# Kernel optimization log

Measured on AMD Instinct MI355X. Metric: run time of the kernel, lower is better.

## Reference

```python
import jax, jax.numpy as jnp
import numpy as np

D, H, KVH, HD, FF = 768, 12, 4, 64, 2048
N_REP = H // KVH
EPS = 1e-6


def rmsnorm(x, w):
    # Faithful to source: norm = ||x|| * n^{-1/2}; eps added to norm (not inside sqrt)
    norm = jnp.sqrt(jnp.sum(x * x, axis=-1, keepdims=True)) * (x.shape[-1] ** -0.5)
    return w * x / (norm + EPS)


def rope_tables(seq_len, head_dim, base=10000.0):
    inv_freq = 1.0 / (base ** (np.arange(0, head_dim, 2, dtype=np.float32) / head_dim))
    t = np.arange(seq_len, dtype=np.float32)
    freqs = np.einsum('i,j->ij', t, inv_freq)  # [S, HD/2]
    emb = np.concatenate([freqs, freqs], axis=-1)  # [S, HD]
    return jnp.asarray(np.cos(emb)), jnp.asarray(np.sin(emb))


def rotate_half(x):
    h = x.shape[-1] // 2
    return jnp.concatenate([-x[..., h:], x[..., :h]], axis=-1)


def setup_inputs() -> dict:
    key = jax.random.key(0)
    ks = jax.random.split(key, 9)
    s = 0.02
    return {
        'x': jax.random.normal(ks[0], (2, 2048, D), jnp.float32),
        'Wq': jax.random.normal(ks[1], (H * HD, D), jnp.float32) * s,
        'Wk': jax.random.normal(ks[2], (KVH * HD, D), jnp.float32) * s,
        'Wv': jax.random.normal(ks[3], (KVH * HD, D), jnp.float32) * s,
        'Wo': jax.random.normal(ks[4], (D, H * HD), jnp.float32) * s,
        'Wgate': jax.random.normal(ks[5], (FF, D), jnp.float32) * s,
        'Wup': jax.random.normal(ks[6], (FF, D), jnp.float32) * s,
        'Wdown': jax.random.normal(ks[7], (D, FF), jnp.float32) * s,
        'g1': jnp.ones((D,), jnp.float32),
        'g2': jnp.ones((D,), jnp.float32),
    }


def reference(x, Wq, Wk, Wv, Wo, Wgate, Wup, Wdown, g1, g2):
    B, S, _ = x.shape
    # ---- attention sublayer (pre-norm) ----
    xn = rmsnorm(x, g1)
    q = (xn @ Wq.T).reshape(B, S, H, HD).transpose(0, 2, 1, 3)      # [B,H,S,HD]
    k = (xn @ Wk.T).reshape(B, S, KVH, HD).transpose(0, 2, 1, 3)    # [B,KVH,S,HD]
    v = (xn @ Wv.T).reshape(B, S, KVH, HD).transpose(0, 2, 1, 3)
    cos, sin = rope_tables(S, HD)                                   # [S,HD]
    q = q * cos + rotate_half(q) * sin
    k = k * cos + rotate_half(k) * sin
    # repeat kv heads to match q heads
    k = jnp.repeat(k, N_REP, axis=1)                                # [B,H,S,HD]
    v = jnp.repeat(v, N_REP, axis=1)
    scores = jnp.einsum('bhqd,bhkd->bhqk', q, k) / jnp.sqrt(jnp.float32(HD))
    causal = jnp.tril(jnp.ones((S, S), bool))
    scores = jnp.where(causal, scores, jnp.finfo(scores.dtype).min)
    attn = jax.nn.softmax(scores, axis=-1)
    out = jnp.einsum('bhqk,bhkd->bhqd', attn, v)                    # [B,H,S,HD]
    out = out.transpose(0, 2, 1, 3).reshape(B, S, H * HD) @ Wo.T
    x = x + out
    # ---- SwiGLU FFN sublayer (pre-norm) ----
    xn2 = rmsnorm(x, g2)
    ff = (jax.nn.silu(xn2 @ Wgate.T) * (xn2 @ Wup.T)) @ Wdown.T
    return x + ff
```

## Files before the change

### kernel.cpp

```cpp
#include <hip/hip_runtime.h>
#include <hip/hip_bf16.h>
#include <math.h>

typedef __bf16 bf16;
typedef __attribute__((ext_vector_type(8))) __bf16 bf16x8;
typedef __attribute__((ext_vector_type(4))) __bf16 bf16x4;
typedef __attribute__((ext_vector_type(4))) float f32x4;

#define MFMA16(a,b,c) __builtin_amdgcn_mfma_f32_16x16x32_bf16(a,b,c,0,0,0)

#define BATCH 2
#define SEQ   2048
#define DMODEL 768
#define NH    12
#define NKV   4
#define NREP  3
#define HD    64
#define FFDIM 2048
#define ROWS  (BATCH*SEQ)

#define QSCALE 0.18033688011112042f
#define LOG2E  1.4426950408889634f

#define WB(N) asm volatile("s_waitcnt vmcnt(" #N ")\n\ts_barrier" ::: "memory")
#define BAR() asm volatile("s_barrier" ::: "memory")

__device__ __forceinline__ void gl2lds16(const bf16* g, bf16* l) {
  __builtin_amdgcn_global_load_lds(
      (const __attribute__((address_space(1))) void*)g,
      (__attribute__((address_space(3))) void*)l, 16, 0, 0);
}

struct Cvt7 { const float* s[7]; bf16* d[7]; int n[7]; float* tab; };
__global__ __launch_bounds__(256) void cvt_all_kernel(Cvt7 c) {
  int seg = blockIdx.y;
  if (seg == 7) {
    int id = blockIdx.x * 256 + threadIdx.x;
    int j = id >> 11, s = id & 2047;
    float inv = expf(-(float)j * (9.210340371976184f / 32.0f));
    float ang = (float)s * inv;
    c.tab[id] = cosf(ang);
    c.tab[65536 + id] = sinf(ang);
    return;
  }
  const float* __restrict__ src = c.s[seg];
  bf16* __restrict__ dst = c.d[seg];
  int n = c.n[seg];
  int stride = gridDim.x * 256;
  for (int i = blockIdx.x * 256 + threadIdx.x; i < n; i += stride)
    dst[i] = (bf16)src[i];
}

__global__ __launch_bounds__(192) void rmsnorm_kernel(const float* __restrict__ x,
    const float* __restrict__ g, bf16* __restrict__ out) {
  int row = blockIdx.x;
  const float* xr = x + (size_t)row * DMODEL;
  int t = threadIdx.x;
  f32x4 v = *(const f32x4*)(xr + t * 4);
  float ss = v[0] * v[0] + v[1] * v[1] + v[2] * v[2] + v[3] * v[3];
  #pragma unroll
  for (int off = 32; off; off >>= 1) ss += __shfl_xor(ss, off, 64);
  __shared__ float red[3];
  if ((t & 63) == 0) red[t >> 6] = ss;
  __syncthreads();
  float total = red[0] + red[1] + red[2];
  float norm = sqrtf(total) * 0.03608439182435161f;
  float sc = 1.0f / (norm + 1e-6f);
  f32x4 gv = *(const f32x4*)(g + t * 4);
  bf16x4 o;
  #pragma unroll
  for (int i = 0; i < 4; ++i) o[i] = (bf16)(gv[i] * v[i] * sc);
  *(bf16x4*)(out + (size_t)row * DMODEL + t * 4) = o;
}

__global__ __launch_bounds__(512, 6) void gemm_out_kernel(const bf16* __restrict__ A,
    const bf16* __restrict__ B, float* __restrict__ C, const float* __restrict__ R,
    int N, int K) {
  __shared__ __align__(16) bf16 At[2][3][64 * 32];
  __shared__ __align__(16) bf16 Bt[2][3][64 * 32];
  int t = threadIdx.x;
  int g = t >> 8;
  int tt = t & 255;
  int lane = t & 63;
  int w = (t >> 6) & 3;
  int l15 = lane & 15, lq = lane >> 4;
  int wrow = (w >> 1) * 32, wcol = (w & 1) * 32;

  int flat = blockIdx.y * 12 + blockIdx.x;
  int f2 = (flat & 7) * 96 + (flat >> 3);
  int col0 = (f2 % 12) * 64, row0 = (f2 / 12) * 64;

  const int KH = K >> 1;
  const int NS = KH / 32;
  const bf16* Ag = A + (size_t)(row0 + (tt >> 2)) * K + g * KH + (tt & 3) * 8;
  const bf16* Bg = B + (size_t)(col0 + (tt >> 2)) * K + g * KH + (tt & 3) * 8;

  #pragma unroll
  for (int s = 0; s < 2; ++s) {
    gl2lds16(Ag + s * 32, At[g][s] + tt * 8);
    gl2lds16(Bg + s * 32, Bt[g][s] + tt * 8);
  }

  f32x4 zero = {0.f, 0.f, 0.f, 0.f};
  f32x4 acc[2][2];
  #pragma unroll
  for (int m = 0; m < 2; ++m)
    #pragma unroll
    for (int n = 0; n < 2; ++n) acc[m][n] = zero;

  #define OG_COMPUTE(slot) do {                                              \
    const bf16* at = At[g][slot]; const bf16* bt = Bt[g][slot];              \
    bf16x8 af[2], bb[2];                                                     \
    _Pragma("unroll")                                                        \
    for (int m = 0; m < 2; ++m)                                              \
      af[m] = *(const bf16x8*)(at + (wrow + m * 16 + l15) * 32 + lq * 8);    \
    _Pragma("unroll")                                                        \
    for (int n = 0; n < 2; ++n)                                              \
      bb[n] = *(const bf16x8*)(bt + (wcol + n * 16 + l15) * 32 + lq * 8);    \
    _Pragma("unroll")                                                        \
    for (int m = 0; m < 2; ++m)                                              \
      _Pragma("unroll")                                                      \
      for (int n = 0; n < 2; ++n)                                            \
        acc[m][n] = MFMA16(af[m], bb[n], acc[m][n]);                         \
  } while (0)

  int slot = 0;
  for (int k = 0; k < NS - 1; ++k) {
    WB(2);
    if (k + 2 < NS) {
      int ks = (k + 2) * 32;
      int ws = slot + 2; if (ws >= 3) ws -= 3;
      gl2lds16(Ag + ks, At[g][ws] + tt * 8);
      gl2lds16(Bg + ks, Bt[g][ws] + tt * 8);
    }
    OG_COMPUTE(slot);
    slot = (slot == 2) ? 0 : slot + 1;
  }
  WB(0);
  OG_COMPUTE(slot);
  #undef OG_COMPUTE

  __syncthreads();
  float* Cl = (float*)&At[0][0][0];
  if (g == 1) {
    #pragma unroll
    for (int m = 0; m < 2; ++m)
      #pragma unroll
      for (int n = 0; n < 2; ++n)
        #pragma unroll
        for (int r = 0; r < 4; ++r)
          Cl[(wrow + m * 16 + lq * 4 + r) * 64 + wcol + n * 16 + l15] = acc[m][n][r];
  }
  __syncthreads();
  if (g == 0) {
    #pragma unroll
    for (int m = 0; m < 2; ++m)
      #pragma unroll
      for (int n = 0; n < 2; ++n)
        #pragma unroll
        for (int r = 0; r < 4; ++r) {
          int row = wrow + m * 16 + lq * 4 + r;
          int col = wcol + n * 16 + l15;
          size_t idx = (size_t)(row0 + row) * N + col0 + col;
          C[idx] = acc[m][n][r] + Cl[row * 64 + col] + R[idx];
        }
  }
}

__global__ __launch_bounds__(256) void gemm_qkv_kernel(const bf16* __restrict__ A,
    const bf16* __restrict__ Wcat, const float* __restrict__ tab,
    bf16* __restrict__ Qh, bf16* __restrict__ Kh, bf16* __restrict__ Vt) {
  __shared__ __align__(16) bf16 At[4][64 * 32];
  __shared__ __align__(16) bf16 Bt[4][128 * 32];
  const int K = DMODEL;
  int t = threadIdx.x, lane = t & 63, wave = t >> 6;
  int l15 = lane & 15, lq = lane >> 4;
  int wrow = (wave >> 1) * 32, wcol = (wave & 1) * 64;
  int row0 = blockIdx.y * 64, col0 = blockIdx.x * 128;
  const bf16* Ag  = A + (size_t)(row0 + (t >> 2)) * K + (t & 3) * 8;
  const bf16* Bg0 = Wcat + (size_t)(col0 + (t >> 2)) * K + (t & 3) * 8;
  const bf16* Bg1 = Bg0 + (size_t)64 * K;
  const int NS = K / 32;

  #pragma unroll
  for (int s = 0; s < 3; ++s) {
    int ks = s * 32;
    gl2lds16(Ag + ks,  At[s] + t * 8);
    gl2lds16(Bg0 + ks, Bt[s] + t * 8);
    gl2lds16(Bg1 + ks, Bt[s] + 2048 + t * 8);
  }

  f32x4 zero = {0.f, 0.f, 0.f, 0.f};
  f32x4 acc[2][4];
  #pragma unroll
  for (int m = 0; m < 2; ++m)
    #pragma unroll
    for (int n = 0; n < 4; ++n) acc[m][n] = zero;

  #define QK_COMPUTE(slot) do {                                              \
    const bf16* at = At[slot]; const bf16* bt = Bt[slot];                    \
    bf16x8 af[2], bfr[4];                                                    \
    _Pragma("unroll")                                                        \
    for (int m = 0; m < 2; ++m)                                              \
      af[m] = *(const bf16x8*)(at + (wrow + m * 16 + l15) * 32 + lq * 8);    \
    _Pragma("unroll")                                                        \
    for (int n = 0; n < 4; ++n)                                              \
      bfr[n] = *(const bf16x8*)(bt + (wcol + n * 16 + l15) * 32 + lq * 8);   \
    _Pragma("unroll")                                                        \
    for (int m = 0; m < 2; ++m)                                              \
      _Pragma("unroll")                                                      \
      for (int n = 0; n < 4; ++n)                                            \
        acc[m][n] = MFMA16(af[m], bfr[n], acc[m][n]);                        \
  } while (0)

  for (int k = 0; k < NS - 2; ++k) {
    WB(6);
    if (k + 3 < NS) {
      int ks = (k + 3) * 32;
      int ws = (k + 3) & 3;
      gl2lds16(Ag + ks,  At[ws] + t * 8);
      gl2lds16(Bg0 + ks, Bt[ws] + t * 8);
      gl2lds16(Bg1 + ks, Bt[ws] + 2048 + t * 8);
    }
    QK_COMPUTE(k & 3);
  }
  WB(3);
  QK_COMPUTE((NS - 2) & 3);
  WB(0);
  QK_COMPUTE((NS - 1) & 3);
  #undef QK_COMPUTE

  int b = row0 >> 11;
  int s0 = (row0 & 2047) + wrow + lq * 4;
  int colw = col0 + wcol;
  if (colw < 768) {
    int h = colw >> 6;
    f32x4 cv[2][2], sv[2][2];
    #pragma unroll
    for (int m = 0; m < 2; ++m)
      #pragma unroll
      for (int jh = 0; jh < 2; ++jh) {
        const float* cp = tab + (jh * 16 + l15) * 2048 + s0 + m * 16;
        cv[m][jh] = *(const f32x4*)cp;
        sv[m][jh] = *(const f32x4*)(cp + 65536);
      }
    #pragma unroll
    for (int m = 0; m < 2; ++m)
      #pragma unroll
      for (int n = 0; n < 4; ++n) {
        float sgn = (n < 2) ? -1.f : 1.f;
        #pragma unroll
        for (int r = 0; r < 4; ++r) {
          float c = cv[m][n & 1][r], si = sv[m][n & 1][r];
          float rp = (acc[m][n][r] * c + sgn * acc[m][n ^ 2][r] * si) * QSCALE;
          Qh[((size_t)(b * NH + h) * SEQ + s0 + m * 16 + r) * 64 + n * 16 + l15] = (bf16)rp;
        }
      }
  } else if (colw < 1024) {
    int kh = (colw - 768) >> 6;
    f32x4 cv[2][2], sv[2][2];
    #pragma unroll
    for (int m = 0; m < 2; ++m)
      #pragma unroll
      for (int jh = 0; jh < 2; ++jh) {
        const float* cp = tab + (jh * 16 + l15) * 2048 + s0 + m * 16;
        cv[m][jh] = *(const f32x4*)cp;
        sv[m][jh] = *(const f32x4*)(cp + 65536);
      }
    #pragma unroll
    for (int m = 0; m < 2; ++m)
      #pragma unroll
      for (int n = 0; n < 4; ++n) {
        float sgn = (n < 2) ? -1.f : 1.f;
        #pragma unroll
        for (int r = 0; r < 4; ++r) {
          float c = cv[m][n & 1][r], si = sv[m][n & 1][r];
          float rp = acc[m][n][r] * c + sgn * acc[m][n ^ 2][r] * si;
          Kh[((size_t)(b * NKV + kh) * SEQ + s0 + m * 16 + r) * 64 + n * 16 + l15] = (bf16)rp;
        }
      }
  } else {
    int vh = (colw - 1024) >> 6;
    #pragma unroll
    for (int m = 0; m < 2; ++m)
      #pragma unroll
      for (int n = 0; n < 4; ++n) {
        bf16x4 pv;
        #pragma unroll
        for (int r = 0; r < 4; ++r) pv[r] = (bf16)acc[m][n][r];
        *(bf16x4*)(Vt + ((size_t)(b * NKV + vh) * 64 + n * 16 + l15) * SEQ + s0 + m * 16) = pv;
      }
  }
}

__global__ __launch_bounds__(256, 2) void gemm_gu_kernel(const bf16* __restrict__ A,
    const bf16* __restrict__ Wg, const bf16* __restrict__ Wu, bf16* __restrict__ H) {
  __shared__ __align__(16) bf16 At[3][128 * 32];
  __shared__ __align__(16) bf16 Bgt[3][128 * 32];
  __shared__ __align__(16) bf16 But[3][128 * 32];
  const int K = DMODEL;
  int t = threadIdx.x, lane = t & 63, wave = t >> 6;
  int l15 = lane & 15, lq = lane >> 4;
  int wrow = (wave >> 1) * 64, wcol = (wave & 1) * 64;
  int row0 = blockIdx.y * 128, col0 = blockIdx.x * 128;
  const bf16* Ag0 = A  + (size_t)(row0 + (t >> 2)) * K + (t & 3) * 8;
  const bf16* Ag1 = Ag0 + (size_t)64 * K;
  const bf16* Gg0 = Wg + (size_t)(col0 + (t >> 2)) * K + (t & 3) * 8;
  const bf16* Gg1 = Gg0 + (size_t)64 * K;
  const bf16* Ug0 = Wu + (size_t)(col0 + (t >> 2)) * K + (t & 3) * 8;
  const bf16* Ug1 = Ug0 + (size_t)64 * K;
  const int NS = K / 32;

  #pragma unroll
  for (int s = 0; s < 2; ++s) {
    int ks = s * 32;
    gl2lds16(Ag0 + ks, At[s] + t * 8);
    gl2lds16(Ag1 + ks, At[s] + 2048 + t * 8);
    gl2lds16(Gg0 + ks, Bgt[s] + t * 8);
    gl2lds16(Gg1 + ks, Bgt[s] + 2048 + t * 8);
    gl2lds16(Ug0 + ks, But[s] + t * 8);
    gl2lds16(Ug1 + ks, But[s] + 2048 + t * 8);
  }

  f32x4 zero = {0.f, 0.f, 0.f, 0.f};
  f32x4 ag[4][4], au[4][4];
  #pragma unroll
  for (int m = 0; m < 4; ++m)
    #pragma unroll
    for (int n = 0; n < 4; ++n) { ag[m][n] = zero; au[m][n] = zero; }

  #define GU_COMPUTE(slot) do {                                              \
    const bf16* at = At[slot];                                               \
    const bf16* bgt = Bgt[slot]; const bf16* but = But[slot];                \
    bf16x8 af[4], bb[4];                                                     \
    _Pragma("unroll")                                                        \
    for (int m = 0; m < 4; ++m)                                              \
      af[m] = *(const bf16x8*)(at + (wrow + m * 16 + l15) * 32 + lq * 8);    \
    _Pragma("unroll")                                                        \
    for (int n = 0; n < 4; ++n)                                              \
      bb[n] = *(const bf16x8*)(bgt + (wcol + n * 16 + l15) * 32 + lq * 8);   \
    _Pragma("unroll")                                                        \
    for (int m = 0; m < 4; ++m)                                              \
      _Pragma("unroll")                                                      \
      for (int n = 0; n < 4; ++n)                                            \
        ag[m][n] = MFMA16(af[m], bb[n], ag[m][n]);                           \
    _Pragma("unroll")                                                        \
    for (int n = 0; n < 4; ++n)                                              \
      bb[n] = *(const bf16x8*)(but + (wcol + n * 16 + l15) * 32 + lq * 8);   \
    _Pragma("unroll")                                                        \
    for (int m = 0; m < 4; ++m)                                              \
      _Pragma("unroll")                                                      \
      for (int n = 0; n < 4; ++n)                                            \
        au[m][n] = MFMA16(af[m], bb[n], au[m][n]);                           \
  } while (0)

  int slot = 0;
  for (int k = 0; k < NS - 1; ++k) {
    WB(6);
    if (k + 2 < NS) {
      int ks = (k + 2) * 32;
      int ws = slot + 2; if (ws >= 3) ws -= 3;
      gl2lds16(Ag0 + ks, At[ws] + t * 8);
      gl2lds16(Ag1 + ks, At[ws] + 2048 + t * 8);
      gl2lds16(Gg0 + ks, Bgt[ws] + t * 8);
      gl2lds16(Gg1 + ks, Bgt[ws] + 2048 + t * 8);
      gl2lds16(Ug0 + ks, But[ws] + t * 8);
      gl2lds16(Ug1 + ks, But[ws] + 2048 + t * 8);
    }
    GU_COMPUTE(slot);
    slot = (slot == 2) ? 0 : slot + 1;
  }
  WB(0);
  GU_COMPUTE(slot);
  #undef GU_COMPUTE

  #pragma unroll
  for (int m = 0; m < 4; ++m)
    #pragma unroll
    for (int n = 0; n < 4; ++n)
      #pragma unroll
      for (int r = 0; r < 4; ++r) {
        int row = row0 + wrow + m * 16 + lq * 4 + r;
        int col = col0 + wcol + n * 16 + l15;
        float g = ag[m][n][r], u = au[m][n][r];
        float sg = g / (1.f + __builtin_amdgcn_exp2f(-g * LOG2E));
        H[(size_t)row * FFDIM + col] = (bf16)(sg * u);
      }
}

__global__ __launch_bounds__(256) void attn_kernel(const bf16* __restrict__ Qh,
    const bf16* __restrict__ Kh, const bf16* __restrict__ Vt, bf16* __restrict__ out) {
  __shared__ __align__(16) bf16 Kl0[2][64 * 32];
  __shared__ __align__(16) bf16 Kl1[2][64 * 32];
  __shared__ __align__(16) bf16 Vl0[2][64 * 32];
  __shared__ __align__(16) bf16 Vl1[2][64 * 32];
  __shared__ __align__(16) bf16 P[4][16 * 80];

  int idx = blockIdx.x;
  int qt = 31 - (idx / 24);
  int bh = idx % 24;
  int q0blk = qt * 64;
  int b = bh / NH, h = bh % NH;
  int kvh = h / NREP;
  int t = threadIdx.x;
  int lane = t & 63, wave = t >> 6;
  int l15 = lane & 15, lq = lane >> 4;
  int qw = q0blk + wave * 16;
  const bf16* Qb = Qh + (size_t)(b * NH + h) * SEQ * 64;
  const bf16* Kb = Kh + (size_t)(b * NKV + kvh) * SEQ * 64;
  const bf16* Vb = Vt + (size_t)(b * NKV + kvh) * 64 * SEQ;

  bf16x8 bq0 = *(const bf16x8*)(Qb + (size_t)(qw + l15) * 64 + lq * 8);
  bf16x8 bq1 = *(const bf16x8*)(Qb + (size_t)(qw + l15) * 64 + 32 + lq * 8);

  const bf16* Kg = Kb + (size_t)(t >> 2) * 64 + (t & 3) * 8;
  const bf16* Vg = Vb + (size_t)(t >> 2) * SEQ + (t & 3) * 8;
  bf16* Pw = P[wave];
  int Pwq = l15 * 80, lq8 = lq * 8, lq4 = lq * 4;
  const int NS = qt + 1;

  #pragma unroll
  for (int s = 0; s < 2; ++s) {
    int ks = (s < NS ? s : NS - 1) * 64;
    gl2lds16(Kg + (size_t)ks * 64,      Kl0[s] + t * 8);
    gl2lds16(Kg + (size_t)ks * 64 + 32, Kl1[s] + t * 8);
    gl2lds16(Vg + ks,                   Vl0[s] + t * 8);
    gl2lds16(Vg + ks + 32,              Vl1[s] + t * 8);
  }

  f32x4 zero = {0.f, 0.f, 0.f, 0.f};
  f32x4 o[4];
  o[0] = zero; o[1] = zero; o[2] = zero; o[3] = zero;
  float l_r = 0.f;

  #define ATTN_STEP(kk, slot) do {                                           \
    int k0 = (kk) * 64;                                                      \
    const bf16* kl0 = Kl0[slot]; const bf16* kl1 = Kl1[slot];                \
    const bf16* vl0 = Vl0[slot]; const bf16* vl1 = Vl1[slot];                \
    f32x4 s[4];                                                              \
    _Pragma("unroll")                                                        \
    for (int c = 0; c < 4; ++c) {                                            \
      bf16x8 ak0 = *(const bf16x8*)(kl0 + (c * 16 + l15) * 32 + lq8);        \
      bf16x8 ak1 = *(const bf16x8*)(kl1 + (c * 16 + l15) * 32 + lq8);        \
      s[c] = zero;                                                           \
      s[c] = MFMA16(ak0, bq0, s[c]);                                         \
      s[c] = MFMA16(ak1, bq1, s[c]);                                         \
    }                                                                        \
    if (k0 + 63 > qw) {                                                      \
      int qmk = qw + l15 - k0 - lq4;                                         \
      _Pragma("unroll")                                                      \
      for (int c = 0; c < 4; ++c)                                            \
        _Pragma("unroll")                                                    \
        for (int r = 0; r < 4; ++r)                                          \
          if (c * 16 + r > qmk) s[c][r] = -INFINITY;                         \
    }                                                                        \
    _Pragma("unroll")                                                        \
    for (int c = 0; c < 4; ++c) {                                            \
      bf16x4 pe;                                                             \
      _Pragma("unroll")                                                      \
      for (int r = 0; r < 4; ++r) {                                          \
        float e = __builtin_amdgcn_exp2f(s[c][r]);                           \
        l_r += e;                                                            \
        pe[r] = (bf16)e;                                                     \
      }                                                                      \
      *(bf16x4*)(Pw + Pwq + c * 16 + lq4) = pe;                              \
    }                                                                        \
    bf16x8 bp0 = *(const bf16x8*)(Pw + Pwq + lq8);                           \
    bf16x8 bp1 = *(const bf16x8*)(Pw + Pwq + 32 + lq8);                      \
    _Pragma("unroll")                                                        \
    for (int n = 0; n < 4; ++n) {                                            \
      bf16x8 av0 = *(const bf16x8*)(vl0 + (n * 16 + l15) * 32 + lq8);        \
      bf16x8 av1 = *(const bf16x8*)(vl1 + (n * 16 + l15) * 32 + lq8);        \
      o[n] = MFMA16(av0, bp0, o[n]);                                         \
      o[n] = MFMA16(av1, bp1, o[n]);                                         \
    }                                                                        \
  } while (0)

  for (int k = 0; k < NS - 1; ++k) {
    WB(4);
    ATTN_STEP(k, k & 1);
    BAR();
    if (k <= NS - 3) {
      int ks = (k + 2) * 64;
      gl2lds16(Kg + (size_t)ks * 64,      Kl0[k & 1] + t * 8);
      gl2lds16(Kg + (size_t)ks * 64 + 32, Kl1[k & 1] + t * 8);
      gl2lds16(Vg + ks,                   Vl0[k & 1] + t * 8);
      gl2lds16(Vg + ks + 32,              Vl1[k & 1] + t * 8);
    }
  }
  {
    WB(0);
    ATTN_STEP(NS - 1, (NS - 1) & 1);
  }
  #undef ATTN_STEP

  float lt = l_r;
  lt += __shfl_xor(lt, 16, 64);
  lt += __shfl_xor(lt, 32, 64);
  float inv = 1.f / lt;
  int q = qw + l15;
  bf16* orow = out + (size_t)(b * SEQ + q) * DMODEL + h * 64;
  #pragma unroll
  for (int n = 0; n < 4; ++n) {
    bf16x4 po;
    #pragma unroll
    for (int r = 0; r < 4; ++r) po[r] = (bf16)(o[n][r] * inv);
    *(bf16x4*)(orow + n * 16 + lq4) = po;
  }
}

extern "C" void kernel_launch(void* const* d_in, const int* in_sizes, int n_in,
                              void* d_out, int out_size, void* d_ws, size_t ws_size,
                              hipStream_t stream) {
  const float* x     = (const float*)d_in[0];
  const float* Wq    = (const float*)d_in[1];
  const float* Wk    = (const float*)d_in[2];
  const float* Wv    = (const float*)d_in[3];
  const float* Wo    = (const float*)d_in[4];
  const float* Wgate = (const float*)d_in[5];
  const float* Wup   = (const float*)d_in[6];
  const float* Wdown = (const float*)d_in[7];
  const float* g1    = (const float*)d_in[8];
  const float* g2    = (const float*)d_in[9];
  float* out = (float*)d_out;

  char* ws = (char*)d_ws;
  size_t off = 0;
  auto alloc = [&](size_t bytes) { size_t o = off; off += (bytes + 255) & ~(size_t)255; return o; };
  size_t o_tab  = alloc((size_t)2 * 32 * 2048 * 4);
  size_t o_x1   = alloc((size_t)4096 * 768 * 4);
  size_t o_xn   = alloc((size_t)4096 * 768 * 2);
  size_t o_Qh   = alloc((size_t)2 * 12 * 2048 * 64 * 2);
  size_t o_Kh   = alloc((size_t)2 * 4 * 2048 * 64 * 2);
  size_t o_Vt   = alloc((size_t)2 * 4 * 64 * 2048 * 2);
  size_t o_ao   = alloc((size_t)4096 * 768 * 2);
  size_t o_H    = alloc((size_t)4096 * 2048 * 2);
  size_t o_Wcat = alloc((size_t)1280 * 768 * 2);
  size_t o_Wo   = alloc((size_t)768 * 768 * 2);
  size_t o_Wgu  = alloc((size_t)4096 * 768 * 2);
  size_t o_Wdn  = alloc((size_t)768 * 2048 * 2);
  if (ws_size < off) return;

  float* tab  = (float*)(ws + o_tab);
  float* fx1  = (float*)(ws + o_x1);
  bf16* bxn   = (bf16*)(ws + o_xn);
  bf16* bQh   = (bf16*)(ws + o_Qh);
  bf16* bKh   = (bf16*)(ws + o_Kh);
  bf16* bVt   = (bf16*)(ws + o_Vt);
  bf16* bao   = (bf16*)(ws + o_ao);
  bf16* bH    = (bf16*)(ws + o_H);
  bf16* bWcat = (bf16*)(ws + o_Wcat);
  bf16* bWo   = (bf16*)(ws + o_Wo);
  bf16* bWgu  = (bf16*)(ws + o_Wgu);
  bf16* bWdn  = (bf16*)(ws + o_Wdn);

  Cvt7 c;
  c.s[0] = Wq;    c.d[0] = bWcat;              c.n[0] = 768 * 768;
  c.s[1] = Wk;    c.d[1] = bWcat + 768 * 768;  c.n[1] = 256 * 768;
  c.s[2] = Wv;    c.d[2] = bWcat + 1024 * 768; c.n[2] = 256 * 768;
  c.s[3] = Wo;    c.d[3] = bWo;                c.n[3] = 768 * 768;
  c.s[4] = Wgate; c.d[4] = bWgu;               c.n[4] = 2048 * 768;
  c.s[5] = Wup;   c.d[5] = bWgu + 2048 * 768;  c.n[5] = 2048 * 768;
  c.s[6] = Wdown; c.d[6] = bWdn;               c.n[6] = 768 * 2048;
  c.tab = tab;
  cvt_all_kernel<<<dim3(256, 8), 256, 0, stream>>>(c);

  rmsnorm_kernel<<<4096, 192, 0, stream>>>(x, g1, bxn);
  gemm_qkv_kernel<<<dim3(10, 64), 256, 0, stream>>>(bxn, bWcat, tab, bQh, bKh, bVt);
  attn_kernel<<<dim3(768), 256, 0, stream>>>(bQh, bKh, bVt, bao);
  gemm_out_kernel<<<dim3(12, 64), 512, 0, stream>>>(bao, bWo, fx1, x, 768, 768);

  rmsnorm_kernel<<<4096, 192, 0, stream>>>(fx1, g2, bxn);
  gemm_gu_kernel<<<dim3(16, 32), 256, 0, stream>>>(bxn, bWgu, bWgu + 2048 * 768, bH);
  gemm_out_kernel<<<dim3(12, 64), 512, 0, stream>>>(bH, bWdn, out, fx1, 768, 2048);
}
```

Measured before the change: 242.7 us.

## Interleave gate/up weights and rewrite gate-up GEMM with 256x256 ping-pong tiles

```diff
diff --git a/kernel.cpp b/kernel.cpp
--- a/kernel.cpp
+++ b/kernel.cpp
@@ -47,6 +47,15 @@
   bf16* __restrict__ dst = c.d[seg];
   int n = c.n[seg];
   int stride = gridDim.x * 256;
+  if (seg == 4 || seg == 5) {
+    int up = (seg == 5) ? 32 : 0;
+    for (int i = blockIdx.x * 256 + threadIdx.x; i < n; i += stride) {
+      int rg = i / 768, cc = i - rg * 768;
+      int drow = ((rg >> 5) << 6) + (rg & 31) + up;
+      dst[(size_t)drow * 768 + cc] = (bf16)src[i];
+    }
+    return;
+  }
   for (int i = blockIdx.x * 256 + threadIdx.x; i < n; i += stride)
     dst[i] = (bf16)src[i];
 }
@@ -293,96 +302,131 @@
   }
 }
 
-__global__ __launch_bounds__(256, 2) void gemm_gu_kernel(const bf16* __restrict__ A,
-    const bf16* __restrict__ Wg, const bf16* __restrict__ Wu, bf16* __restrict__ H) {
-  __shared__ __align__(16) bf16 At[3][128 * 32];
-  __shared__ __align__(16) bf16 Bgt[3][128 * 32];
-  __shared__ __align__(16) bf16 But[3][128 * 32];
-  const int K = DMODEL;
+__global__ __launch_bounds__(512, 2) void gemm_gu_kernel(const bf16* __restrict__ A,
+    const bf16* __restrict__ W, bf16* __restrict__ H) {
+  __shared__ __align__(16) bf16 Als[2 * 2 * 128 * 64];
+  __shared__ __align__(16) bf16 Bls[2 * 2 * 128 * 64];
+  const int NT = 12;
   int t = threadIdx.x, lane = t & 63, wave = t >> 6;
-  int l15 = lane & 15, lq = lane >> 4;
-  int wrow = (wave >> 1) * 64, wcol = (wave & 1) * 64;
-  int row0 = blockIdx.y * 128, col0 = blockIdx.x * 128;
-  const bf16* Ag0 = A  + (size_t)(row0 + (t >> 2)) * K + (t & 3) * 8;
-  const bf16* Ag1 = Ag0 + (size_t)64 * K;
-  const bf16* Gg0 = Wg + (size_t)(col0 + (t >> 2)) * K + (t & 3) * 8;
-  const bf16* Gg1 = Gg0 + (size_t)64 * K;
-  const bf16* Ug0 = Wu + (size_t)(col0 + (t >> 2)) * K + (t & 3) * 8;
-  const bf16* Ug1 = Ug0 + (size_t)64 * K;
-  const int NS = K / 32;
-
-  #pragma unroll
-  for (int s = 0; s < 2; ++s) {
-    int ks = s * 32;
-    gl2lds16(Ag0 + ks, At[s] + t * 8);
-    gl2lds16(Ag1 + ks, At[s] + 2048 + t * 8);
-    gl2lds16(Gg0 + ks, Bgt[s] + t * 8);
-    gl2lds16(Gg1 + ks, Bgt[s] + 2048 + t * 8);
-    gl2lds16(Ug0 + ks, But[s] + t * 8);
-    gl2lds16(Ug1 + ks, But[s] + 2048 + t * 8);
-  }
+  int l15 = lane & 15, lq = lane >> 4, lq8 = lq * 8;
+  int wm = wave >> 2, wn = wave & 3;
+
+  int flat = blockIdx.y * 16 + blockIdx.x;
+  int f2 = (flat & 7) * 32 + (flat >> 3);
+  int colb = f2 & 15, rowb = f2 >> 4;
+  int row0 = rowb * 256, col0w = colb * 256;
+
+  #define STAGE(G, orow, L, j, h) do {                                       \
+    bf16* lb = (L) + ((j) & 1) * 16384 + (h) * 8192 + (t >> 3) * 64 + (t & 7) * 8; \
+    const bf16* gb = (G) + (size_t)((orow) + (h) * 128 + (t >> 3)) * 768     \
+                   + (j) * 64 + (t & 7) * 8;                                 \
+    gl2lds16(gb, lb);                                                        \
+    gl2lds16(gb + (size_t)64 * 768, lb + 64 * 64);                           \
+  } while (0)
+
+  STAGE(W, col0w, Bls, 0, 0);  STAGE(W, col0w, Bls, 0, 1);
+  STAGE(A, row0,  Als, 0, 0);  STAGE(A, row0,  Als, 0, 1);
+  STAGE(W, col0w, Bls, 1, 0);  STAGE(W, col0w, Bls, 1, 1);
 
   f32x4 zero = {0.f, 0.f, 0.f, 0.f};
-  f32x4 ag[4][4], au[4][4];
-  #pragma unroll
-  for (int m = 0; m < 4; ++m)
-    #pragma unroll
-    for (int n = 0; n < 4; ++n) { ag[m][n] = zero; au[m][n] = zero; }
-
-  #define GU_COMPUTE(slot) do {                                              \
-    const bf16* at = At[slot];                                               \
-    const bf16* bgt = Bgt[slot]; const bf16* but = But[slot];                \
-    bf16x8 af[4], bb[4];                                                     \
-    _Pragma("unroll")                                                        \
-    for (int m = 0; m < 4; ++m)                                              \
-      af[m] = *(const bf16x8*)(at + (wrow + m * 16 + l15) * 32 + lq * 8);    \
-    _Pragma("unroll")                                                        \
-    for (int n = 0; n < 4; ++n)                                              \
-      bb[n] = *(const bf16x8*)(bgt + (wcol + n * 16 + l15) * 32 + lq * 8);   \
-    _Pragma("unroll")                                                        \
-    for (int m = 0; m < 4; ++m)                                              \
-      _Pragma("unroll")                                                      \
-      for (int n = 0; n < 4; ++n)                                            \
-        ag[m][n] = MFMA16(af[m], bb[n], ag[m][n]);                           \
-    _Pragma("unroll")                                                        \
-    for (int n = 0; n < 4; ++n)                                              \
-      bb[n] = *(const bf16x8*)(but + (wcol + n * 16 + l15) * 32 + lq * 8);   \
-    _Pragma("unroll")                                                        \
-    for (int m = 0; m < 4; ++m)                                              \
-      _Pragma("unroll")                                                      \
-      for (int n = 0; n < 4; ++n)                                            \
-        au[m][n] = MFMA16(af[m], bb[n], au[m][n]);                           \
-  } while (0)
-
-  int slot = 0;
-  for (int k = 0; k < NS - 1; ++k) {
-    WB(6);
-    if (k + 2 < NS) {
-      int ks = (k + 2) * 32;
-      int ws = slot + 2; if (ws >= 3) ws -= 3;
-      gl2lds16(Ag0 + ks, At[ws] + t * 8);
-      gl2lds16(Ag1 + ks, At[ws] + 2048 + t * 8);
-      gl2lds16(Gg0 + ks, Bgt[ws] + t * 8);
-      gl2lds16(Gg1 + ks, Bgt[ws] + 2048 + t * 8);
-      gl2lds16(Ug0 + ks, But[ws] + t * 8);
-      gl2lds16(Ug1 + ks, But[ws] + 2048 + t * 8);
-    }
-    GU_COMPUTE(slot);
-    slot = (slot == 2) ? 0 : slot + 1;
-  }
-  WB(0);
-  GU_COMPUTE(slot);
-  #undef GU_COMPUTE
-
-  #pragma unroll
-  for (int m = 0; m < 4; ++m)
-    #pragma unroll
-    for (int n = 0; n < 4; ++n)
+  f32x4 acc[8][4];
+  #pragma unroll
+  for (int m = 0; m < 8; ++m)
+    #pragma unroll
+    for (int n = 0; n < 4; ++n) acc[m][n] = zero;
+
+  WB(4);
+
+  for (int j = 0; j < NT; ++j) {
+    const bf16* aB = Als + (j & 1) * 16384 + wm * 8192;
+    const bf16* bB = Bls + (j & 1) * 16384 + (wn >> 1) * 8192 + (wn & 1) * 4096;
+    bf16x8 afr[4][2], bfr[4][2];
+
+    #pragma unroll
+    for (int m = 0; m < 4; ++m)
+      #pragma unroll
+      for (int kk = 0; kk < 2; ++kk)
+        afr[m][kk] = *(const bf16x8*)(aB + (m * 16 + l15) * 64 + kk * 32 + lq8);
+    #pragma unroll
+    for (int n = 0; n < 2; ++n)
+      #pragma unroll
+      for (int kk = 0; kk < 2; ++kk)
+        bfr[n][kk] = *(const bf16x8*)(bB + (n * 16 + l15) * 64 + kk * 32 + lq8);
+    if (j + 1 < NT) STAGE(A, row0, Als, j + 1, 0);
+    BAR();
+    __builtin_amdgcn_s_setprio(1);
+    #pragma unroll
+    for (int m = 0; m < 4; ++m)
+      #pragma unroll
+      for (int n = 0; n < 2; ++n) {
+        acc[m][n] = MFMA16(afr[m][0], bfr[n][0], acc[m][n]);
+        acc[m][n] = MFMA16(afr[m][1], bfr[n][1], acc[m][n]);
+      }
+    __builtin_amdgcn_s_setprio(0);
+    BAR();
+
+    #pragma unroll
+    for (int n = 2; n < 4; ++n)
+      #pragma unroll
+      for (int kk = 0; kk < 2; ++kk)
+        bfr[n][kk] = *(const bf16x8*)(bB + (n * 16 + l15) * 64 + kk * 32 + lq8);
+    if (j + 1 < NT) STAGE(A, row0, Als, j + 1, 1);
+    BAR();
+    __builtin_amdgcn_s_setprio(1);
+    #pragma unroll
+    for (int m = 0; m < 4; ++m)
+      #pragma unroll
+      for (int n = 2; n < 4; ++n) {
+        acc[m][n] = MFMA16(afr[m][0], bfr[n][0], acc[m][n]);
+        acc[m][n] = MFMA16(afr[m][1], bfr[n][1], acc[m][n]);
+      }
+    __builtin_amdgcn_s_setprio(0);
+    BAR();
+
+    #pragma unroll
+    for (int m = 0; m < 4; ++m)
+      #pragma unroll
+      for (int kk = 0; kk < 2; ++kk)
+        afr[m][kk] = *(const bf16x8*)(aB + ((m + 4) * 16 + l15) * 64 + kk * 32 + lq8);
+    if (j + 2 < NT) STAGE(W, col0w, Bls, j + 2, 0);
+    BAR();
+    __builtin_amdgcn_s_setprio(1);
+    #pragma unroll
+    for (int m = 0; m < 4; ++m)
+      #pragma unroll
+      for (int n = 0; n < 2; ++n) {
+        acc[m + 4][n] = MFMA16(afr[m][0], bfr[n][0], acc[m + 4][n]);
+        acc[m + 4][n] = MFMA16(afr[m][1], bfr[n][1], acc[m + 4][n]);
+      }
+    __builtin_amdgcn_s_setprio(0);
+    BAR();
+
+    if (j + 2 < NT) STAGE(W, col0w, Bls, j + 2, 1);
+    BAR();
+    __builtin_amdgcn_s_setprio(1);
+    #pragma unroll
+    for (int m = 0; m < 4; ++m)
+      #pragma unroll
+      for (int n = 2; n < 4; ++n) {
+        acc[m + 4][n] = MFMA16(afr[m][0], bfr[n][0], acc[m + 4][n]);
+        acc[m + 4][n] = MFMA16(afr[m][1], bfr[n][1], acc[m + 4][n]);
+      }
+    __builtin_amdgcn_s_setprio(0);
+    if (j < NT - 2)       WB(4);
+    else if (j == NT - 2) WB(0);
+  }
+  #undef STAGE
+
+  int hc0 = colb * 128 + wn * 32;
+  #pragma unroll
+  for (int m = 0; m < 8; ++m)
+    #pragma unroll
+    for (int n = 0; n < 2; ++n)
       #pragma unroll
       for (int r = 0; r < 4; ++r) {
-        int row = row0 + wrow + m * 16 + lq * 4 + r;
-        int col = col0 + wcol + n * 16 + l15;
-        float g = ag[m][n][r], u = au[m][n][r];
+        int row = row0 + wm * 128 + m * 16 + lq * 4 + r;
+        int col = hc0 + n * 16 + l15;
+        float g = acc[m][n][r], u = acc[m][n + 2][r];
         float sg = g / (1.f + __builtin_amdgcn_exp2f(-g * LOG2E));
         H[(size_t)row * FFDIM + col] = (bf16)(sg * u);
       }
@@ -560,7 +604,7 @@
   c.s[2] = Wv;    c.d[2] = bWcat + 1024 * 768; c.n[2] = 256 * 768;
   c.s[3] = Wo;    c.d[3] = bWo;                c.n[3] = 768 * 768;
   c.s[4] = Wgate; c.d[4] = bWgu;               c.n[4] = 2048 * 768;
-  c.s[5] = Wup;   c.d[5] = bWgu + 2048 * 768;  c.n[5] = 2048 * 768;
+  c.s[5] = Wup;   c.d[5] = bWgu;               c.n[5] = 2048 * 768;
   c.s[6] = Wdown; c.d[6] = bWdn;               c.n[6] = 768 * 2048;
   c.tab = tab;
   cvt_all_kernel<<<dim3(256, 8), 256, 0, stream>>>(c);
@@ -571,6 +615,6 @@
   gemm_out_kernel<<<dim3(12, 64), 512, 0, stream>>>(bao, bWo, fx1, x, 768, 768);
 
   rmsnorm_kernel<<<4096, 192, 0, stream>>>(fx1, g2, bxn);
-  gemm_gu_kernel<<<dim3(16, 32), 256, 0, stream>>>(bxn, bWgu, bWgu + 2048 * 768, bH);
+  gemm_gu_kernel<<<dim3(16, 16), 512, 0, stream>>>(bxn, bWgu, bH);
   gemm_out_kernel<<<dim3(12, 64), 512, 0, stream>>>(bH, bWdn, out, fx1, 768, 2048);
 }
```

New measurement: 246.5 us. Within noise of the previous version (+1.6%).

## Interleave gate/up weights into one matrix and swizzle LDS staging rows

Applied to the files above, without the earlier changes.

```diff
diff --git a/kernel.cpp b/kernel.cpp
--- a/kernel.cpp
+++ b/kernel.cpp
@@ -47,6 +47,15 @@
   bf16* __restrict__ dst = c.d[seg];
   int n = c.n[seg];
   int stride = gridDim.x * 256;
+  if (seg == 4 || seg == 5) {
+    int up = (seg == 5) ? 32 : 0;
+    for (int i = blockIdx.x * 256 + threadIdx.x; i < n; i += stride) {
+      int rg = i / 768, cc = i - rg * 768;
+      int drow = ((rg >> 5) << 6) + (rg & 31) + up;
+      dst[(size_t)drow * 768 + cc] = (bf16)src[i];
+    }
+    return;
+  }
   for (int i = blockIdx.x * 256 + threadIdx.x; i < n; i += stride)
     dst[i] = (bf16)src[i];
 }
@@ -294,78 +303,62 @@
 }
 
 __global__ __launch_bounds__(256, 2) void gemm_gu_kernel(const bf16* __restrict__ A,
-    const bf16* __restrict__ Wg, const bf16* __restrict__ Wu, bf16* __restrict__ H) {
-  __shared__ __align__(16) bf16 At[3][128 * 32];
-  __shared__ __align__(16) bf16 Bgt[3][128 * 32];
-  __shared__ __align__(16) bf16 But[3][128 * 32];
-  const int K = DMODEL;
+    const bf16* __restrict__ W, bf16* __restrict__ H) {
+  __shared__ __align__(16) bf16 Als[3][128 * 32];
+  __shared__ __align__(16) bf16 Bls[3][128 * 32];
+  const int NS = 24;
   int t = threadIdx.x, lane = t & 63, wave = t >> 6;
   int l15 = lane & 15, lq = lane >> 4;
-  int wrow = (wave >> 1) * 64, wcol = (wave & 1) * 64;
-  int row0 = blockIdx.y * 128, col0 = blockIdx.x * 128;
-  const bf16* Ag0 = A  + (size_t)(row0 + (t >> 2)) * K + (t & 3) * 8;
-  const bf16* Ag1 = Ag0 + (size_t)64 * K;
-  const bf16* Gg0 = Wg + (size_t)(col0 + (t >> 2)) * K + (t & 3) * 8;
-  const bf16* Gg1 = Gg0 + (size_t)64 * K;
-  const bf16* Ug0 = Wu + (size_t)(col0 + (t >> 2)) * K + (t & 3) * 8;
-  const bf16* Ug1 = Ug0 + (size_t)64 * K;
-  const int NS = K / 32;
-
-  #pragma unroll
-  for (int s = 0; s < 2; ++s) {
-    int ks = s * 32;
-    gl2lds16(Ag0 + ks, At[s] + t * 8);
-    gl2lds16(Ag1 + ks, At[s] + 2048 + t * 8);
-    gl2lds16(Gg0 + ks, Bgt[s] + t * 8);
-    gl2lds16(Gg1 + ks, Bgt[s] + 2048 + t * 8);
-    gl2lds16(Ug0 + ks, But[s] + t * 8);
-    gl2lds16(Ug1 + ks, But[s] + 2048 + t * 8);
-  }
+  int lfrag = l15 * 32 + lq * 8;
+  int wm = wave >> 1, wn = wave & 1;
+
+  int flat = blockIdx.y * 32 + blockIdx.x;
+  int f2 = (flat & 7) * 128 + (flat >> 3);
+  int colb = f2 & 31, rowb = f2 >> 5;
+  int row0 = rowb * 128, col0w = colb * 128;
+
+  #define STAGE(G, orow, L, slot, j) do {                                    \
+    bf16* lb = (L)[slot] + t * 8;                                            \
+    const bf16* gb = (G) + (size_t)((orow) + ((t >> 6) << 4)                 \
+                   + ((t >> 2) & 15)) * 768 + (j) * 32 + (t & 3) * 8;        \
+    gl2lds16(gb, lb);                                                        \
+    gl2lds16(gb + (size_t)64 * 768, lb + 2048);                              \
+  } while (0)
+
+  STAGE(A, row0,  Als, 0, 0);  STAGE(W, col0w, Bls, 0, 0);
+  STAGE(A, row0,  Als, 1, 1);  STAGE(W, col0w, Bls, 1, 1);
 
   f32x4 zero = {0.f, 0.f, 0.f, 0.f};
-  f32x4 ag[4][4], au[4][4];
+  f32x4 acc[4][4];
   #pragma unroll
   for (int m = 0; m < 4; ++m)
     #pragma unroll
-    for (int n = 0; n < 4; ++n) { ag[m][n] = zero; au[m][n] = zero; }
+    for (int n = 0; n < 4; ++n) acc[m][n] = zero;
 
   #define GU_COMPUTE(slot) do {                                              \
-    const bf16* at = At[slot];                                               \
-    const bf16* bgt = Bgt[slot]; const bf16* but = But[slot];                \
+    const bf16* aB = Als[slot] + lfrag;                                      \
+    const bf16* bB = Bls[slot] + lfrag;                                      \
     bf16x8 af[4], bb[4];                                                     \
     _Pragma("unroll")                                                        \
     for (int m = 0; m < 4; ++m)                                              \
-      af[m] = *(const bf16x8*)(at + (wrow + m * 16 + l15) * 32 + lq * 8);    \
+      af[m] = *(const bf16x8*)(aB + (wm * 4 + m) * 512);                     \
     _Pragma("unroll")                                                        \
     for (int n = 0; n < 4; ++n)                                              \
-      bb[n] = *(const bf16x8*)(bgt + (wcol + n * 16 + l15) * 32 + lq * 8);   \
+      bb[n] = *(const bf16x8*)(bB + (wn * 4 + n) * 512);                     \
     _Pragma("unroll")                                                        \
     for (int m = 0; m < 4; ++m)                                              \
       _Pragma("unroll")                                                      \
       for (int n = 0; n < 4; ++n)                                            \
-        ag[m][n] = MFMA16(af[m], bb[n], ag[m][n]);                           \
-    _Pragma("unroll")                                                        \
-    for (int n = 0; n < 4; ++n)                                              \
-      bb[n] = *(const bf16x8*)(but + (wcol + n * 16 + l15) * 32 + lq * 8);   \
-    _Pragma("unroll")                                                        \
-    for (int m = 0; m < 4; ++m)                                              \
-      _Pragma("unroll")                                                      \
-      for (int n = 0; n < 4; ++n)                                            \
-        au[m][n] = MFMA16(af[m], bb[n], au[m][n]);                           \
+        acc[m][n] = MFMA16(af[m], bb[n], acc[m][n]);                         \
   } while (0)
 
   int slot = 0;
   for (int k = 0; k < NS - 1; ++k) {
-    WB(6);
+    WB(4);
     if (k + 2 < NS) {
-      int ks = (k + 2) * 32;
       int ws = slot + 2; if (ws >= 3) ws -= 3;
-      gl2lds16(Ag0 + ks, At[ws] + t * 8);
-      gl2lds16(Ag1 + ks, At[ws] + 2048 + t * 8);
-      gl2lds16(Gg0 + ks, Bgt[ws] + t * 8);
-      gl2lds16(Gg1 + ks, Bgt[ws] + 2048 + t * 8);
-      gl2lds16(Ug0 + ks, But[ws] + t * 8);
-      gl2lds16(Ug1 + ks, But[ws] + 2048 + t * 8);
+      STAGE(A, row0,  Als, ws, k + 2);
+      STAGE(W, col0w, Bls, ws, k + 2);
     }
     GU_COMPUTE(slot);
     slot = (slot == 2) ? 0 : slot + 1;
@@ -373,16 +366,18 @@
   WB(0);
   GU_COMPUTE(slot);
   #undef GU_COMPUTE
-
+  #undef STAGE
+
+  int hc0 = colb * 64 + wn * 32;
   #pragma unroll
   for (int m = 0; m < 4; ++m)
     #pragma unroll
-    for (int n = 0; n < 4; ++n)
+    for (int n = 0; n < 2; ++n)
       #pragma unroll
       for (int r = 0; r < 4; ++r) {
-        int row = row0 + wrow + m * 16 + lq * 4 + r;
-        int col = col0 + wcol + n * 16 + l15;
-        float g = ag[m][n][r], u = au[m][n][r];
+        int row = row0 + wm * 64 + m * 16 + lq * 4 + r;
+        int col = hc0 + n * 16 + l15;
+        float g = acc[m][n][r], u = acc[m][n + 2][r];
         float sg = g / (1.f + __builtin_amdgcn_exp2f(-g * LOG2E));
         H[(size_t)row * FFDIM + col] = (bf16)(sg * u);
       }
@@ -413,10 +408,13 @@
   bf16x8 bq0 = *(const bf16x8*)(Qb + (size_t)(qw + l15) * 64 + lq * 8);
   bf16x8 bq1 = *(const bf16x8*)(Qb + (size_t)(qw + l15) * 64 + 32 + lq * 8);
 
-  const bf16* Kg = Kb + (size_t)(t >> 2) * 64 + (t & 3) * 8;
-  const bf16* Vg = Vb + (size_t)(t >> 2) * SEQ + (t & 3) * 8;
+  int srow = (t >> 6) * 16 + ((t >> 2) & 15);
+  int scol = (t & 3) * 8;
+  const bf16* Kg = Kb + (size_t)srow * 64 + scol;
+  const bf16* Vg = Vb + (size_t)srow * SEQ + scol;
   bf16* Pw = P[wave];
   int Pwq = l15 * 80, lq8 = lq * 8, lq4 = lq * 4;
+  int lfrag = l15 * 32 + lq8;
   const int NS = qt + 1;
 
   #pragma unroll
@@ -440,8 +438,8 @@
     f32x4 s[4];                                                              \
     _Pragma("unroll")                                                        \
     for (int c = 0; c < 4; ++c) {                                            \
-      bf16x8 ak0 = *(const bf16x8*)(kl0 + (c * 16 + l15) * 32 + lq8);        \
-      bf16x8 ak1 = *(const bf16x8*)(kl1 + (c * 16 + l15) * 32 + lq8);        \
+      bf16x8 ak0 = *(const bf16x8*)(kl0 + c * 512 + lfrag);                  \
+      bf16x8 ak1 = *(const bf16x8*)(kl1 + c * 512 + lfrag);                  \
       s[c] = zero;                                                           \
       s[c] = MFMA16(ak0, bq0, s[c]);                                         \
       s[c] = MFMA16(ak1, bq1, s[c]);                                         \
@@ -469,8 +467,8 @@
     bf16x8 bp1 = *(const bf16x8*)(Pw + Pwq + 32 + lq8);                      \
     _Pragma("unroll")                                                        \
     for (int n = 0; n < 4; ++n) {                                            \
-      bf16x8 av0 = *(const bf16x8*)(vl0 + (n * 16 + l15) * 32 + lq8);        \
-      bf16x8 av1 = *(const bf16x8*)(vl1 + (n * 16 + l15) * 32 + lq8);        \
+      bf16x8 av0 = *(const bf16x8*)(vl0 + n * 512 + lfrag);                  \
+      bf16x8 av1 = *(const bf16x8*)(vl1 + n * 512 + lfrag);                  \
       o[n] = MFMA16(av0, bp0, o[n]);                                         \
       o[n] = MFMA16(av1, bp1, o[n]);                                         \
     }                                                                        \
@@ -560,7 +558,7 @@
   c.s[2] = Wv;    c.d[2] = bWcat + 1024 * 768; c.n[2] = 256 * 768;
   c.s[3] = Wo;    c.d[3] = bWo;                c.n[3] = 768 * 768;
   c.s[4] = Wgate; c.d[4] = bWgu;               c.n[4] = 2048 * 768;
-  c.s[5] = Wup;   c.d[5] = bWgu + 2048 * 768;  c.n[5] = 2048 * 768;
+  c.s[5] = Wup;   c.d[5] = bWgu;               c.n[5] = 2048 * 768;
   c.s[6] = Wdown; c.d[6] = bWdn;               c.n[6] = 768 * 2048;
   c.tab = tab;
   cvt_all_kernel<<<dim3(256, 8), 256, 0, stream>>>(c);
@@ -571,6 +569,6 @@
   gemm_out_kernel<<<dim3(12, 64), 512, 0, stream>>>(bao, bWo, fx1, x, 768, 768);
 
   rmsnorm_kernel<<<4096, 192, 0, stream>>>(fx1, g2, bxn);
-  gemm_gu_kernel<<<dim3(16, 32), 256, 0, stream>>>(bxn, bWgu, bWgu + 2048 * 768, bH);
+  gemm_gu_kernel<<<dim3(32, 32), 256, 0, stream>>>(bxn, bWgu, bH);
   gemm_out_kernel<<<dim3(12, 64), 512, 0, stream>>>(bH, bWdn, out, fx1, 768, 2048);
 }
```

Measured after the change: 257.0 us. +5.9%, slower.
